# Performance work log

Measured on AMD Instinct MI355X. Metric: run time of the kernel, lower is better.

## Reference

```python
import jax, jax.numpy as jnp
import numpy as np

B, CI, CO, H, W, M1, M2 = 4, 64, 64, 256, 256, 16, 16


def setup_inputs() -> dict:
    key = jax.random.key(0)
    k0, k1, k2, k3, k4 = jax.random.split(key, 5)
    scale = 1.0 / (CI * CO)
    x = jax.random.normal(k0, (B, CI, H, W), dtype=jnp.float32)
    # torch.rand -> uniform [0,1), scaled; real/imag parts of complex weights
    w1r = scale * jax.random.uniform(k1, (CO, CI, M1, M2), dtype=jnp.float32)
    w1i = scale * jax.random.uniform(k2, (CO, CI, M1, M2), dtype=jnp.float32)
    w2r = scale * jax.random.uniform(k3, (CO, CI, M1, M2), dtype=jnp.float32)
    w2i = scale * jax.random.uniform(k4, (CO, CI, M1, M2), dtype=jnp.float32)
    return {"x": x, "w1r": w1r, "w1i": w1i, "w2r": w2r, "w2i": w2i}


def reference(x, w1r, w1i, w2r, w2i):
    b, ci, h, w = x.shape
    co, _, m1, m2 = w1r.shape
    wf = w // 2 + 1  # rfft width
    x_ft = jnp.fft.rfft2(x)                       # [b, ci, h, wf] complex
    xs = x_ft[:, :, :m1, :m2]                     # low-frequency slice
    w1 = w1r + 1j * w1i
    w2 = w2r + 1j * w2i
    o1 = jnp.einsum('bixy,ioxy->boxy', xs, w1)    # [b, co, m1, m2]
    o2 = jnp.einsum('bixy,ioxy->boxy', xs, w2)    # same slice, per original code
    out_ft = jnp.zeros((b, co, h, wf), dtype=x_ft.dtype)
    out_ft = out_ft.at[:, :, :m1, :m2].set(o1)
    out_ft = out_ft.at[:, :, h - m1:, :m2].set(o2)
    return jnp.fft.irfft2(out_ft, s=(h, w))
```

## Files before the change

### kernel.cpp

```cpp
#include <hip/hip_runtime.h>

#define NB 4
#define NCI 64
#define NCO 64
#define PLANE 65536

#define OF_XS_RE 0
#define OF_XS_IM (OF_XS_RE + PLANE)
#define OF_O1_RE (OF_XS_IM + PLANE)
#define OF_O1_IM (OF_O1_RE + PLANE)
#define OF_O2_RE (OF_O1_IM + PLANE)
#define OF_O2_IM (OF_O2_RE + PLANE)

#define XEOFF(w) ((w)*260)
#define XOOFF(w) (16*260 + 8 + (w)*260)

#define TPF 6.2831853071795864769f

__global__ __launch_bounds__(1024, 4) void k12_dft(const float* __restrict__ x,
                                                   float* __restrict__ ws) {
  __shared__ float bufA[8336], bufB[8336];
  __shared__ float cst[256], snt[256];
  __shared__ float2 s2[1024];
  const int t = threadIdx.x;
  const int img = blockIdx.x;

  if (t < 256) {
    float sv_, cv_;
    sincosf(TPF * (float)t * (1.0f/256.0f), &sv_, &cv_);
    cst[t] = cv_;  snt[t] = sv_;
  }

  const int sl = t & 3, row = t >> 2;
  const int wq = t & 3, p = (t >> 2) & 1;
  const int kg = (t >> 3) & 1, tr = t >> 4;
  int kyv[4];
#pragma unroll
  for (int j = 0; j < 4; ++j) kyv[j] = p + 8*kg + 2*j;

  const float* xb = x + (size_t)img * 65536;

  float4 lo = *(const float4*)(xb + row*256 + sl*4);
  float4 hi = *(const float4*)(xb + row*256 + 128 + sl*4);

  __syncthreads();

  float cd[4], sd[4];
#pragma unroll
  for (int j = 0; j < 4; ++j) { cd[j] = cst[kyv[j]]; sd[j] = snt[kyv[j]]; }

  float ar[4][4], ai[4][4];
#pragma unroll
  for (int j = 0; j < 4; ++j)
#pragma unroll
    for (int r = 0; r < 4; ++r) { ar[j][r] = 0.f; ai[j][r] = 0.f; }

  bufA[XEOFF(sl*4+0) + row] = lo.x + hi.x;
  bufA[XEOFF(sl*4+1) + row] = lo.y + hi.y;
  bufA[XEOFF(sl*4+2) + row] = lo.z + hi.z;
  bufA[XEOFF(sl*4+3) + row] = lo.w + hi.w;
  bufA[XOOFF(sl*4+0) + row] = lo.x - hi.x;
  bufA[XOOFF(sl*4+1) + row] = lo.y - hi.y;
  bufA[XOOFF(sl*4+2) + row] = lo.z - hi.z;
  bufA[XOOFF(sl*4+3) + row] = lo.w - hi.w;
  __syncthreads();

  const int pofs = p ? (16*260 + 8) : 0;

  for (int c = 0; c < 8; ++c) {
    float* cur = (c & 1) ? bufB : bufA;
    float* nxt = (c & 1) ? bufA : bufB;
    if (c < 7) {
      const int w0n = (c+1) * 16;
      lo = *(const float4*)(xb + row*256 + w0n + sl*4);
      hi = *(const float4*)(xb + row*256 + w0n + 128 + sl*4);
    }
    float cc[4], sv[4];
#pragma unroll
    for (int j = 0; j < 4; ++j) {
      const int m = (kyv[j] * (c*16 + wq*4)) & 255;
      cc[j] = cst[m];
      sv[j] = snt[m];
    }
    const float* rp = cur + pofs;
#pragma unroll
    for (int i = 0; i < 4; ++i) {
      const int wl = wq*4 + i;
      const float4 xs4 = *(const float4*)&rp[wl*260 + tr*4];
#pragma unroll
      for (int j = 0; j < 4; ++j) {
        ar[j][0] += xs4.x * cc[j];  ai[j][0] -= xs4.x * sv[j];
        ar[j][1] += xs4.y * cc[j];  ai[j][1] -= xs4.y * sv[j];
        ar[j][2] += xs4.z * cc[j];  ai[j][2] -= xs4.z * sv[j];
        ar[j][3] += xs4.w * cc[j];  ai[j][3] -= xs4.w * sv[j];
        const float nc = cc[j]*cd[j] - sv[j]*sd[j];
        const float ns = sv[j]*cd[j] + cc[j]*sd[j];
        cc[j] = nc; sv[j] = ns;
      }
    }
    if (c < 7) {
      nxt[XEOFF(sl*4+0) + row] = lo.x + hi.x;
      nxt[XEOFF(sl*4+1) + row] = lo.y + hi.y;
      nxt[XEOFF(sl*4+2) + row] = lo.z + hi.z;
      nxt[XEOFF(sl*4+3) + row] = lo.w + hi.w;
      nxt[XOOFF(sl*4+0) + row] = lo.x - hi.x;
      nxt[XOOFF(sl*4+1) + row] = lo.y - hi.y;
      nxt[XOOFF(sl*4+2) + row] = lo.z - hi.z;
      nxt[XOOFF(sl*4+3) + row] = lo.w - hi.w;
    }
    __syncthreads();
  }

#pragma unroll
  for (int j = 0; j < 4; ++j)
#pragma unroll
    for (int r = 0; r < 4; ++r) {
      ar[j][r] += __shfl_xor(ar[j][r], 1);
      ar[j][r] += __shfl_xor(ar[j][r], 2);
      ai[j][r] += __shfl_xor(ai[j][r], 1);
      ai[j][r] += __shfl_xor(ai[j][r], 2);
    }
  if (wq == 0) {
#pragma unroll
    for (int j = 0; j < 4; ++j) {
      const int ky = kyv[j];
      float4 sr; sr.x = ar[j][0]; sr.y = ar[j][1]; sr.z = ar[j][2]; sr.w = ar[j][3];
      float4 si; si.x = ai[j][0]; si.y = ai[j][1]; si.z = ai[j][2]; si.w = ai[j][3];
      *(float4*)&bufA[XEOFF(ky) + tr*4] = sr;
      *(float4*)&bufA[XOOFF(ky) + tr*4] = si;
    }
  }
  __syncthreads();

  const int ky2 = t & 15, kx = (t >> 4) & 15, hh = t >> 8;
  const float cdk = cst[kx], sdk = snt[kx];
  const int m0 = (kx * hh * 64) & 255;
  float cR = cst[m0], sR = snt[m0];
  float arr = 0.f, aii = 0.f;
  const int be = XEOFF(ky2) + hh*64;
  const int bo = XOOFF(ky2) + hh*64;
#pragma unroll 4
  for (int hq = 0; hq < 16; ++hq) {
    const float4 xr = *(const float4*)&bufA[be + hq*4];
    const float4 xi = *(const float4*)&bufA[bo + hq*4];
    {
      arr += xr.x*cR + xi.x*sR;  aii += xi.x*cR - xr.x*sR;
      const float nc = cR*cdk - sR*sdk, ns = sR*cdk + cR*sdk; cR = nc; sR = ns;
    }
    {
      arr += xr.y*cR + xi.y*sR;  aii += xi.y*cR - xr.y*sR;
      const float nc = cR*cdk - sR*sdk, ns = sR*cdk + cR*sdk; cR = nc; sR = ns;
    }
    {
      arr += xr.z*cR + xi.z*sR;  aii += xi.z*cR - xr.z*sR;
      const float nc = cR*cdk - sR*sdk, ns = sR*cdk + cR*sdk; cR = nc; sR = ns;
    }
    {
      arr += xr.w*cR + xi.w*sR;  aii += xi.w*cR - xr.w*sR;
      const float nc = cR*cdk - sR*sdk, ns = sR*cdk + cR*sdk; cR = nc; sR = ns;
    }
  }
  s2[t].x = arr; s2[t].y = aii;
  __syncthreads();
  if (t < 256) {
    float xre = s2[t].x + s2[t+256].x + s2[t+512].x + s2[t+768].x;
    float xim = s2[t].y + s2[t+256].y + s2[t+512].y + s2[t+768].y;
    ws[OF_XS_RE + img*256 + t] = xre;
    ws[OF_XS_IM + img*256 + t] = xim;
  }
}

__global__ __launch_bounds__(256) void k3_mix(const float* __restrict__ w1r,
    const float* __restrict__ w1i, const float* __restrict__ w2r,
    const float* __restrict__ w2i, float* __restrict__ ws) {
  const int o  = blockIdx.x;
  const int mc = blockIdx.y;
  const int t  = threadIdx.x;
  const int b  = t >> 6;
  const int m  = (mc << 6) + (t & 63);
  const float* xsr = ws + OF_XS_RE;
  const float* xsi = ws + OF_XS_IM;
  float a1r=0.f, a1i=0.f, a2r=0.f, a2i=0.f;
#pragma unroll 4
  for (int i = 0; i < NCI; ++i) {
    const float xr = xsr[((b*NCI + i) << 8) + m];
    const float xi = xsi[((b*NCI + i) << 8) + m];
    const int wi = ((i*NCO + o) << 8) + m;
    const float p = w1r[wi], q = w1i[wi], u = w2r[wi], v = w2i[wi];
    a1r += xr*p - xi*q;
    a1i += xr*q + xi*p;
    a2r += xr*u - xi*v;
    a2i += xr*v + xi*u;
  }
  const int oi = ((b*NCO + o) << 8) + m;
  ws[OF_O1_RE + oi] = a1r;
  ws[OF_O1_IM + oi] = a1i;
  ws[OF_O2_RE + oi] = a2r;
  ws[OF_O2_IM + oi] = a2i;
}

__global__ __launch_bounds__(256) void k45_idft(const float* __restrict__ ws,
                                                float* __restrict__ out) {
  __shared__ __align__(16) float o1r[256], o1i[256], o2r[256], o2i[256];
  __shared__ float cst[256], snt[256];
  __shared__ __align__(16) float Sr[64][20], Si[64][20];
  const int t  = threadIdx.x;
  const int bo = blockIdx.x >> 2;
  const int hc = blockIdx.x & 3;

  o1r[t] = ws[OF_O1_RE + bo*256 + t];
  o1i[t] = ws[OF_O1_IM + bo*256 + t];
  o2r[t] = ws[OF_O2_RE + bo*256 + t];
  o2i[t] = ws[OF_O2_IM + bo*256 + t];
  {
    float sv_, cv_;
    sincosf(TPF * (float)t * (1.0f/256.0f), &sv_, &cv_);
    cst[t] = cv_;  snt[t] = sv_;
  }
  __syncthreads();

  const int wl = t & 31;
  float c[15], s[15], c2[15], s2[15];
#pragma unroll
  for (int k = 0; k < 15; ++k) {
    const int mi = ((k+1) * wl) & 255;
    c[k] = cst[mi];
    s[k] = snt[mi];
  }
  {
    const float R = 0.70710678118654752f;
#pragma unroll
    for (int k = 0; k < 15; ++k) {
      const int r8 = (k + 1) & 7;
      switch (r8) {
        case 0: c2[k] =  c[k];            s2[k] =  s[k];            break;
        case 1: c2[k] = (c[k]-s[k])*R;    s2[k] = (s[k]+c[k])*R;    break;
        case 2: c2[k] = -s[k];            s2[k] =  c[k];            break;
        case 3: c2[k] = -(c[k]+s[k])*R;   s2[k] = (c[k]-s[k])*R;    break;
        case 4: c2[k] = -c[k];            s2[k] = -s[k];            break;
        case 5: c2[k] = (s[k]-c[k])*R;    s2[k] = -(c[k]+s[k])*R;   break;
        case 6: c2[k] =  s[k];            s2[k] = -c[k];            break;
        default:c2[k] = (c[k]+s[k])*R;    s2[k] = (s[k]-c[k])*R;    break;
      }
    }
  }

  {
    const int hl = t >> 2, kq = t & 3;
    const int h  = hc*64 + hl;
    const float chh = cst[h], shh = snt[h];
    float c1 = 1.f, s1 = 0.f;
    const int m2i = (240 * h) & 255;
    float cB = cst[m2i], sB = snt[m2i];
    float4 sr = {0.f,0.f,0.f,0.f}, si = {0.f,0.f,0.f,0.f};
    for (int j = 0; j < 16; ++j) {
      const float4 r1 = *(const float4*)&o1r[j*16 + kq*4];
      const float4 i1 = *(const float4*)&o1i[j*16 + kq*4];
      const float4 r2 = *(const float4*)&o2r[j*16 + kq*4];
      const float4 i2 = *(const float4*)&o2i[j*16 + kq*4];
      sr.x += r1.x*c1 - i1.x*s1 + r2.x*cB - i2.x*sB;
      si.x += r1.x*s1 + i1.x*c1 + r2.x*sB + i2.x*cB;
      sr.y += r1.y*c1 - i1.y*s1 + r2.y*cB - i2.y*sB;
      si.y += r1.y*s1 + i1.y*c1 + r2.y*sB + i2.y*cB;
      sr.z += r1.z*c1 - i1.z*s1 + r2.z*cB - i2.z*sB;
      si.z += r1.z*s1 + i1.z*c1 + r2.z*sB + i2.z*cB;
      sr.w += r1.w*c1 - i1.w*s1 + r2.w*cB - i2.w*sB;
      si.w += r1.w*s1 + i1.w*c1 + r2.w*sB + i2.w*cB;
      const float n1c = c1*chh - s1*shh, n1s = s1*chh + c1*shh;
      const float n2c = cB*chh - sB*shh, n2s = sB*chh + cB*shh;
      c1 = n1c; s1 = n1s; cB = n2c; sB = n2s;
    }
    *(float4*)&Sr[hl][kq*4] = sr;
    *(float4*)&Si[hl][kq*4] = si;
  }
  __syncthreads();

  const int half = (t >> 5) & 1;
  const int wv = t >> 6;
  const float scale = 2.0f / 65536.0f;
  const size_t tilebase = ((size_t)bo*256 + hc*64) * 256;
#pragma unroll 2
  for (int pr = 0; pr < 8; ++pr) {
    const int hl = wv*16 + pr*2 + half;
    const float4 a0 = *(const float4*)&Sr[hl][0];
    const float4 a1 = *(const float4*)&Sr[hl][4];
    const float4 a2 = *(const float4*)&Sr[hl][8];
    const float4 a3 = *(const float4*)&Sr[hl][12];
    const float4 b0 = *(const float4*)&Si[hl][0];
    const float4 b1 = *(const float4*)&Si[hl][4];
    const float4 b2 = *(const float4*)&Si[hl][8];
    const float4 b3 = *(const float4*)&Si[hl][12];
    const float re[16] = {a0.x,a0.y,a0.z,a0.w, a1.x,a1.y,a1.z,a1.w,
                          a2.x,a2.y,a2.z,a2.w, a3.x,a3.y,a3.z,a3.w};
    const float im[16] = {b0.x,b0.y,b0.z,b0.w, b1.x,b1.y,b1.z,b1.w,
                          b2.x,b2.y,b2.z,b2.w, b3.x,b3.y,b3.z,b3.w};
    const size_t ob = tilebase + (size_t)hl*256;

#pragma unroll
    for (int g = 0; g < 2; ++g) {
      const float* cc = g ? c2 : c;
      const float* ss = g ? s2 : s;
      float PA = 0.5f * re[0];
      float PB = 0.f, PC = 0.f, PD = 0.f, QB = 0.f, QD = 0.f;
#pragma unroll
      for (int k = 0; k < 15; ++k) {
        const int ky = k + 1;
        const float R = re[ky], I = im[ky];
        const int cls = ky & 3;
        if (cls == 0)      PA += R*cc[k] - I*ss[k];
        else if (cls == 1) { PB += R*cc[k] - I*ss[k];  QB += R*ss[k] + I*cc[k]; }
        else if (cls == 2) PC += R*cc[k] - I*ss[k];
        else               { PD += R*cc[k] - I*ss[k];  QD += R*ss[k] + I*cc[k]; }
      }
      const float T1 = PA + PC, T2 = PB + PD;
      const float T3 = PA - PC, T4 = QB - QD;
      const int cb = wl + g*32;
      out[ob + cb]       = (T1 + T2) * scale;
      out[ob + cb + 64]  = (T3 - T4) * scale;
      out[ob + cb + 128] = (T1 - T2) * scale;
      out[ob + cb + 192] = (T3 + T4) * scale;
    }
  }
}

extern "C" void kernel_launch(void* const* d_in, const int* in_sizes, int n_in,
                              void* d_out, int out_size, void* d_ws, size_t ws_size,
                              hipStream_t stream) {
  const float* x   = (const float*)d_in[0];
  const float* w1r = (const float*)d_in[1];
  const float* w1i = (const float*)d_in[2];
  const float* w2r = (const float*)d_in[3];
  const float* w2i = (const float*)d_in[4];
  float* out = (float*)d_out;
  float* ws  = (float*)d_ws;

  hipLaunchKernelGGL(k12_dft,  dim3(256),   dim3(1024), 0, stream, x, ws);
  hipLaunchKernelGGL(k3_mix,   dim3(64, 4), dim3(256),  0, stream, w1r, w1i, w2r, w2i, ws);
  hipLaunchKernelGGL(k45_idft, dim3(1024),  dim3(256),  0, stream, ws, out);
}
```

Before: 60.51 us.

## Split forward DFT per image into two row-halves with partial sums

The forward DFT kernel now launches two 512-thread blocks per image, each handling 128 rows, instead of one 1024-thread block per image. Each half writes a partial low-frequency spectrum to its own workspace plane, and the mixing kernel adds the two partials as it loads them. This doubles the block count to 512 across the GPU's CUs, which should improve occupancy and load balance. The cost is extra workspace traffic and doubled activation reads in the mixing kernel.

Result: no change. 61.16 us (+1.1%).

```diff
diff --git a/kernel.cpp b/kernel.cpp
--- a/kernel.cpp
+++ b/kernel.cpp
@@ -5,25 +5,30 @@
 #define NCO 64
 #define PLANE 65536
 
-#define OF_XS_RE 0
-#define OF_XS_IM (OF_XS_RE + PLANE)
-#define OF_O1_RE (OF_XS_IM + PLANE)
+#define OF_XS0_RE 0
+#define OF_XS0_IM (OF_XS0_RE + PLANE)
+#define OF_XS1_RE (2*PLANE)
+#define OF_XS1_IM (3*PLANE)
+#define OF_O1_RE (4*PLANE)
 #define OF_O1_IM (OF_O1_RE + PLANE)
 #define OF_O2_RE (OF_O1_IM + PLANE)
 #define OF_O2_IM (OF_O2_RE + PLANE)
 
-#define XEOFF(w) ((w)*260)
-#define XOOFF(w) (16*260 + 8 + (w)*260)
+#define PL2 132
+#define XE2(w) ((w)*PL2)
+#define XO2(w) (16*PL2 + 8 + (w)*PL2)
 
 #define TPF 6.2831853071795864769f
 
-__global__ __launch_bounds__(1024, 4) void k12_dft(const float* __restrict__ x,
-                                                   float* __restrict__ ws) {
-  __shared__ float bufA[8336], bufB[8336];
+__global__ __launch_bounds__(512, 4) void k12_dft(const float* __restrict__ x,
+                                                  float* __restrict__ ws) {
+  __shared__ float bufA[4232], bufB[4232];
   __shared__ float cst[256], snt[256];
-  __shared__ float2 s2[1024];
+  __shared__ float2 s2[512];
   const int t = threadIdx.x;
-  const int img = blockIdx.x;
+  const int img  = blockIdx.x >> 1;
+  const int half = blockIdx.x & 1;
+  const int r0   = half << 7;
 
   if (t < 256) {
     float sv_, cv_;
@@ -38,7 +43,7 @@
 #pragma unroll
   for (int j = 0; j < 4; ++j) kyv[j] = p + 8*kg + 2*j;
 
-  const float* xb = x + (size_t)img * 65536;
+  const float* xb = x + (size_t)img * 65536 + (size_t)r0 * 256;
 
   float4 lo = *(const float4*)(xb + row*256 + sl*4);
   float4 hi = *(const float4*)(xb + row*256 + 128 + sl*4);
@@ -55,17 +60,17 @@
 #pragma unroll
     for (int r = 0; r < 4; ++r) { ar[j][r] = 0.f; ai[j][r] = 0.f; }
 
-  bufA[XEOFF(sl*4+0) + row] = lo.x + hi.x;
-  bufA[XEOFF(sl*4+1) + row] = lo.y + hi.y;
-  bufA[XEOFF(sl*4+2) + row] = lo.z + hi.z;
-  bufA[XEOFF(sl*4+3) + row] = lo.w + hi.w;
-  bufA[XOOFF(sl*4+0) + row] = lo.x - hi.x;
-  bufA[XOOFF(sl*4+1) + row] = lo.y - hi.y;
-  bufA[XOOFF(sl*4+2) + row] = lo.z - hi.z;
-  bufA[XOOFF(sl*4+3) + row] = lo.w - hi.w;
-  __syncthreads();
-
-  const int pofs = p ? (16*260 + 8) : 0;
+  bufA[XE2(sl*4+0) + row] = lo.x + hi.x;
+  bufA[XE2(sl*4+1) + row] = lo.y + hi.y;
+  bufA[XE2(sl*4+2) + row] = lo.z + hi.z;
+  bufA[XE2(sl*4+3) + row] = lo.w + hi.w;
+  bufA[XO2(sl*4+0) + row] = lo.x - hi.x;
+  bufA[XO2(sl*4+1) + row] = lo.y - hi.y;
+  bufA[XO2(sl*4+2) + row] = lo.z - hi.z;
+  bufA[XO2(sl*4+3) + row] = lo.w - hi.w;
+  __syncthreads();
+
+  const int pofs = p ? (16*PL2 + 8) : 0;
 
   for (int c = 0; c < 8; ++c) {
     float* cur = (c & 1) ? bufB : bufA;
@@ -86,7 +91,7 @@
 #pragma unroll
     for (int i = 0; i < 4; ++i) {
       const int wl = wq*4 + i;
-      const float4 xs4 = *(const float4*)&rp[wl*260 + tr*4];
+      const float4 xs4 = *(const float4*)&rp[wl*PL2 + tr*4];
 #pragma unroll
       for (int j = 0; j < 4; ++j) {
         ar[j][0] += xs4.x * cc[j];  ai[j][0] -= xs4.x * sv[j];
@@ -99,14 +104,14 @@
       }
     }
     if (c < 7) {
-      nxt[XEOFF(sl*4+0) + row] = lo.x + hi.x;
-      nxt[XEOFF(sl*4+1) + row] = lo.y + hi.y;
-      nxt[XEOFF(sl*4+2) + row] = lo.z + hi.z;
-      nxt[XEOFF(sl*4+3) + row] = lo.w + hi.w;
-      nxt[XOOFF(sl*4+0) + row] = lo.x - hi.x;
-      nxt[XOOFF(sl*4+1) + row] = lo.y - hi.y;
-      nxt[XOOFF(sl*4+2) + row] = lo.z - hi.z;
-      nxt[XOOFF(sl*4+3) + row] = lo.w - hi.w;
+      nxt[XE2(sl*4+0) + row] = lo.x + hi.x;
+      nxt[XE2(sl*4+1) + row] = lo.y + hi.y;
+      nxt[XE2(sl*4+2) + row] = lo.z + hi.z;
+      nxt[XE2(sl*4+3) + row] = lo.w + hi.w;
+      nxt[XO2(sl*4+0) + row] = lo.x - hi.x;
+      nxt[XO2(sl*4+1) + row] = lo.y - hi.y;
+      nxt[XO2(sl*4+2) + row] = lo.z - hi.z;
+      nxt[XO2(sl*4+3) + row] = lo.w - hi.w;
     }
     __syncthreads();
   }
@@ -126,19 +131,19 @@
       const int ky = kyv[j];
       float4 sr; sr.x = ar[j][0]; sr.y = ar[j][1]; sr.z = ar[j][2]; sr.w = ar[j][3];
       float4 si; si.x = ai[j][0]; si.y = ai[j][1]; si.z = ai[j][2]; si.w = ai[j][3];
-      *(float4*)&bufA[XEOFF(ky) + tr*4] = sr;
-      *(float4*)&bufA[XOOFF(ky) + tr*4] = si;
+      *(float4*)&bufA[XE2(ky) + tr*4] = sr;
+      *(float4*)&bufA[XO2(ky) + tr*4] = si;
     }
   }
   __syncthreads();
 
   const int ky2 = t & 15, kx = (t >> 4) & 15, hh = t >> 8;
   const float cdk = cst[kx], sdk = snt[kx];
-  const int m0 = (kx * hh * 64) & 255;
+  const int m0 = (kx * (r0 + hh*64)) & 255;
   float cR = cst[m0], sR = snt[m0];
   float arr = 0.f, aii = 0.f;
-  const int be = XEOFF(ky2) + hh*64;
-  const int bo = XOOFF(ky2) + hh*64;
+  const int be = XE2(ky2) + hh*64;
+  const int bo = XO2(ky2) + hh*64;
 #pragma unroll 4
   for (int hq = 0; hq < 16; ++hq) {
     const float4 xr = *(const float4*)&bufA[be + hq*4];
@@ -163,10 +168,11 @@
   s2[t].x = arr; s2[t].y = aii;
   __syncthreads();
   if (t < 256) {
-    float xre = s2[t].x + s2[t+256].x + s2[t+512].x + s2[t+768].x;
-    float xim = s2[t].y + s2[t+256].y + s2[t+512].y + s2[t+768].y;
-    ws[OF_XS_RE + img*256 + t] = xre;
-    ws[OF_XS_IM + img*256 + t] = xim;
+    const float xre = s2[t].x + s2[t+256].x;
+    const float xim = s2[t].y + s2[t+256].y;
+    const int base = half ? OF_XS1_RE : OF_XS0_RE;
+    ws[base + img*256 + t]         = xre;
+    ws[base + PLANE + img*256 + t] = xim;
   }
 }
 
@@ -178,13 +184,12 @@
   const int t  = threadIdx.x;
   const int b  = t >> 6;
   const int m  = (mc << 6) + (t & 63);
-  const float* xsr = ws + OF_XS_RE;
-  const float* xsi = ws + OF_XS_IM;
   float a1r=0.f, a1i=0.f, a2r=0.f, a2i=0.f;
 #pragma unroll 4
   for (int i = 0; i < NCI; ++i) {
-    const float xr = xsr[((b*NCI + i) << 8) + m];
-    const float xi = xsi[((b*NCI + i) << 8) + m];
+    const int idx = ((b*NCI + i) << 8) + m;
+    const float xr = ws[OF_XS0_RE + idx] + ws[OF_XS1_RE + idx];
+    const float xi = ws[OF_XS0_IM + idx] + ws[OF_XS1_IM + idx];
     const int wi = ((i*NCO + o) << 8) + m;
     const float p = w1r[wi], q = w1i[wi], u = w2r[wi], v = w2i[wi];
     a1r += xr*p - xi*q;
@@ -334,7 +339,7 @@
   float* out = (float*)d_out;
   float* ws  = (float*)d_ws;
 
-  hipLaunchKernelGGL(k12_dft,  dim3(256),   dim3(1024), 0, stream, x, ws);
-  hipLaunchKernelGGL(k3_mix,   dim3(64, 4), dim3(256),  0, stream, w1r, w1i, w2r, w2i, ws);
-  hipLaunchKernelGGL(k45_idft, dim3(1024),  dim3(256),  0, stream, ws, out);
+  hipLaunchKernelGGL(k12_dft,  dim3(512),   dim3(512), 0, stream, x, ws);
+  hipLaunchKernelGGL(k3_mix,   dim3(64, 4), dim3(256), 0, stream, w1r, w1i, w2r, w2i, ws);
+  hipLaunchKernelGGL(k45_idft, dim3(1024),  dim3(256), 0, stream, ws, out);
 }
```

## Exploit h/h+128 symmetry in inverse column DFT to halve per-block work

Applied to the files above, without the earlier changes.

The inverse DFT kernel now splits the 16-term column sum into even and odd frequency parts, then forms rows h and h+128 as their sum and difference, since the odd twiddles flip sign at h+128. Each block covers 128 output rows, and the grid is halved to 512 blocks. This removes half of the column DFT arithmetic and twiddle recurrences. In exchange each block uses more shared memory and does more row-stage work, and there are fewer blocks to spread across the device.

New measurement: 57.63 us. -4.8%, faster.

```diff
diff --git a/kernel.cpp b/kernel.cpp
--- a/kernel.cpp
+++ b/kernel.cpp
@@ -203,10 +203,10 @@
                                                 float* __restrict__ out) {
   __shared__ __align__(16) float o1r[256], o1i[256], o2r[256], o2i[256];
   __shared__ float cst[256], snt[256];
-  __shared__ __align__(16) float Sr[64][20], Si[64][20];
-  const int t  = threadIdx.x;
-  const int bo = blockIdx.x >> 2;
-  const int hc = blockIdx.x & 3;
+  __shared__ __align__(16) float Sr[128][20], Si[128][20];
+  const int t   = threadIdx.x;
+  const int bo  = blockIdx.x >> 1;
+  const int hcc = blockIdx.x & 1;
 
   o1r[t] = ws[OF_O1_RE + bo*256 + t];
   o1i[t] = ws[OF_O1_IM + bo*256 + t];
@@ -216,6 +216,47 @@
     float sv_, cv_;
     sincosf(TPF * (float)t * (1.0f/256.0f), &sv_, &cv_);
     cst[t] = cv_;  snt[t] = sv_;
+  }
+  __syncthreads();
+
+  {
+    const int hl = t >> 2, kq = t & 3;
+    const int h  = hcc*64 + hl;
+    const float chh = cst[h], shh = snt[h];
+    float c1 = 1.f, s1 = 0.f;
+    const int m2i = (240 * h) & 255;
+    float cB = cst[m2i], sB = snt[m2i];
+    float4 srE = {0,0,0,0}, siE = {0,0,0,0};
+    float4 srO = {0,0,0,0}, siO = {0,0,0,0};
+#pragma unroll
+    for (int j = 0; j < 16; ++j) {
+      const float4 r1 = *(const float4*)&o1r[j*16 + kq*4];
+      const float4 i1 = *(const float4*)&o1i[j*16 + kq*4];
+      const float4 r2 = *(const float4*)&o2r[j*16 + kq*4];
+      const float4 i2 = *(const float4*)&o2i[j*16 + kq*4];
+      float4& sr = (j & 1) ? srO : srE;
+      float4& si = (j & 1) ? siO : siE;
+      sr.x += r1.x*c1 - i1.x*s1 + r2.x*cB - i2.x*sB;
+      si.x += r1.x*s1 + i1.x*c1 + r2.x*sB + i2.x*cB;
+      sr.y += r1.y*c1 - i1.y*s1 + r2.y*cB - i2.y*sB;
+      si.y += r1.y*s1 + i1.y*c1 + r2.y*sB + i2.y*cB;
+      sr.z += r1.z*c1 - i1.z*s1 + r2.z*cB - i2.z*sB;
+      si.z += r1.z*s1 + i1.z*c1 + r2.z*sB + i2.z*cB;
+      sr.w += r1.w*c1 - i1.w*s1 + r2.w*cB - i2.w*sB;
+      si.w += r1.w*s1 + i1.w*c1 + r2.w*sB + i2.w*cB;
+      const float n1c = c1*chh - s1*shh, n1s = s1*chh + c1*shh;
+      const float n2c = cB*chh - sB*shh, n2s = sB*chh + cB*shh;
+      c1 = n1c; s1 = n1s; cB = n2c; sB = n2s;
+    }
+    float4 sp, sm;
+    sp.x = srE.x + srO.x; sp.y = srE.y + srO.y; sp.z = srE.z + srO.z; sp.w = srE.w + srO.w;
+    sm.x = srE.x - srO.x; sm.y = srE.y - srO.y; sm.z = srE.z - srO.z; sm.w = srE.w - srO.w;
+    *(float4*)&Sr[hl][kq*4]      = sp;
+    *(float4*)&Sr[hl+64][kq*4]   = sm;
+    sp.x = siE.x + siO.x; sp.y = siE.y + siO.y; sp.z = siE.z + siO.z; sp.w = siE.w + siO.w;
+    sm.x = siE.x - siO.x; sm.y = siE.y - siO.y; sm.z = siE.z - siO.z; sm.w = siE.w - siO.w;
+    *(float4*)&Si[hl][kq*4]      = sp;
+    *(float4*)&Si[hl+64][kq*4]   = sm;
   }
   __syncthreads();
 
@@ -245,56 +286,27 @@
     }
   }
 
-  {
-    const int hl = t >> 2, kq = t & 3;
-    const int h  = hc*64 + hl;
-    const float chh = cst[h], shh = snt[h];
-    float c1 = 1.f, s1 = 0.f;
-    const int m2i = (240 * h) & 255;
-    float cB = cst[m2i], sB = snt[m2i];
-    float4 sr = {0.f,0.f,0.f,0.f}, si = {0.f,0.f,0.f,0.f};
-    for (int j = 0; j < 16; ++j) {
-      const float4 r1 = *(const float4*)&o1r[j*16 + kq*4];
-      const float4 i1 = *(const float4*)&o1i[j*16 + kq*4];
-      const float4 r2 = *(const float4*)&o2r[j*16 + kq*4];
-      const float4 i2 = *(const float4*)&o2i[j*16 + kq*4];
-      sr.x += r1.x*c1 - i1.x*s1 + r2.x*cB - i2.x*sB;
-      si.x += r1.x*s1 + i1.x*c1 + r2.x*sB + i2.x*cB;
-      sr.y += r1.y*c1 - i1.y*s1 + r2.y*cB - i2.y*sB;
-      si.y += r1.y*s1 + i1.y*c1 + r2.y*sB + i2.y*cB;
-      sr.z += r1.z*c1 - i1.z*s1 + r2.z*cB - i2.z*sB;
-      si.z += r1.z*s1 + i1.z*c1 + r2.z*sB + i2.z*cB;
-      sr.w += r1.w*c1 - i1.w*s1 + r2.w*cB - i2.w*sB;
-      si.w += r1.w*s1 + i1.w*c1 + r2.w*sB + i2.w*cB;
-      const float n1c = c1*chh - s1*shh, n1s = s1*chh + c1*shh;
-      const float n2c = cB*chh - sB*shh, n2s = sB*chh + cB*shh;
-      c1 = n1c; s1 = n1s; cB = n2c; sB = n2s;
-    }
-    *(float4*)&Sr[hl][kq*4] = sr;
-    *(float4*)&Si[hl][kq*4] = si;
-  }
-  __syncthreads();
-
   const int half = (t >> 5) & 1;
   const int wv = t >> 6;
   const float scale = 2.0f / 65536.0f;
-  const size_t tilebase = ((size_t)bo*256 + hc*64) * 256;
+  const size_t base256 = (size_t)bo*256 + hcc*64;
 #pragma unroll 2
-  for (int pr = 0; pr < 8; ++pr) {
-    const int hl = wv*16 + pr*2 + half;
-    const float4 a0 = *(const float4*)&Sr[hl][0];
-    const float4 a1 = *(const float4*)&Sr[hl][4];
-    const float4 a2 = *(const float4*)&Sr[hl][8];
-    const float4 a3 = *(const float4*)&Sr[hl][12];
-    const float4 b0 = *(const float4*)&Si[hl][0];
-    const float4 b1 = *(const float4*)&Si[hl][4];
-    const float4 b2 = *(const float4*)&Si[hl][8];
-    const float4 b3 = *(const float4*)&Si[hl][12];
+  for (int pr = 0; pr < 16; ++pr) {
+    const int lr = wv*32 + pr*2 + half;
+    const float4 a0 = *(const float4*)&Sr[lr][0];
+    const float4 a1 = *(const float4*)&Sr[lr][4];
+    const float4 a2 = *(const float4*)&Sr[lr][8];
+    const float4 a3 = *(const float4*)&Sr[lr][12];
+    const float4 b0 = *(const float4*)&Si[lr][0];
+    const float4 b1 = *(const float4*)&Si[lr][4];
+    const float4 b2 = *(const float4*)&Si[lr][8];
+    const float4 b3 = *(const float4*)&Si[lr][12];
     const float re[16] = {a0.x,a0.y,a0.z,a0.w, a1.x,a1.y,a1.z,a1.w,
                           a2.x,a2.y,a2.z,a2.w, a3.x,a3.y,a3.z,a3.w};
     const float im[16] = {b0.x,b0.y,b0.z,b0.w, b1.x,b1.y,b1.z,b1.w,
                           b2.x,b2.y,b2.z,b2.w, b3.x,b3.y,b3.z,b3.w};
-    const size_t ob = tilebase + (size_t)hl*256;
+    const int grow = (lr & 63) + ((lr >> 6) << 7);
+    const size_t ob = (base256 + grow) * 256;
 
 #pragma unroll
     for (int g = 0; g < 2; ++g) {
@@ -336,5 +348,5 @@
 
   hipLaunchKernelGGL(k12_dft,  dim3(256),   dim3(1024), 0, stream, x, ws);
   hipLaunchKernelGGL(k3_mix,   dim3(64, 4), dim3(256),  0, stream, w1r, w1i, w2r, w2i, ws);
-  hipLaunchKernelGGL(k45_idft, dim3(1024),  dim3(256),  0, stream, ws, out);
+  hipLaunchKernelGGL(k45_idft, dim3(512),   dim3(256),  0, stream, ws, out);
 }
```
